# Performance work log

Measured on AMD Instinct MI355X. Metric: run time of the kernel, lower is better.

The kernel has to match this reference:

```python
import jax, jax.numpy as jnp
import numpy as np

B, S = 64, 32
C_IN, H, W = 4, 84, 84
D_MODEL, D_STATE, D_CONV, EXPAND = 128, 32, 4, 2
D_INNER = EXPAND * D_MODEL  # 256
DT_RANK = D_MODEL // 16     # 8
CNN_OUT = 64 * 7 * 7        # 3136
FC1, FC2, NA = 128, 128, 18


def setup_inputs() -> dict:
    key = jax.random.key(0)
    ks = jax.random.split(key, 24)
    def g(k, shape, scale=0.02):
        return jax.random.normal(k, shape, dtype=jnp.float32) * scale
    return {
        "x": jax.random.uniform(ks[0], (B, S, C_IN, H, W), dtype=jnp.float32) * 255.0,
        "conv1_w": g(ks[1], (32, C_IN, 8, 8)), "conv1_b": g(ks[2], (32,)),
        "conv2_w": g(ks[3], (64, 32, 4, 4)), "conv2_b": g(ks[4], (64,)),
        "conv3_w": g(ks[5], (64, 64, 3, 3)), "conv3_b": g(ks[6], (64,)),
        "feat_w": g(ks[7], (D_MODEL, CNN_OUT)), "feat_b": g(ks[8], (D_MODEL,)),
        "in_proj_w": g(ks[9], (2 * D_INNER, D_MODEL)),
        "conv1d_w": g(ks[10], (D_INNER, 1, D_CONV)), "conv1d_b": g(ks[11], (D_INNER,)),
        "x_proj_w": g(ks[12], (DT_RANK + 2 * D_STATE, D_INNER)),
        "dt_proj_w": g(ks[13], (D_INNER, DT_RANK), 0.1),
        "dt_proj_b": g(ks[14], (D_INNER,), 0.5),
        "A_log": jnp.log(jnp.tile(jnp.arange(1, D_STATE + 1, dtype=jnp.float32), (D_INNER, 1))),
        "D": jnp.ones((D_INNER,), jnp.float32),
        "out_proj_w": g(ks[15], (D_MODEL, D_INNER)),
        "fc1_w": g(ks[16], (FC1, D_MODEL)), "fc1_b": g(ks[17], (FC1,)),
        "fc2_w": g(ks[18], (FC2, FC1)), "fc2_b": g(ks[19], (FC2,)),
        "q_w": g(ks[20], (NA, FC2)), "q_b": g(ks[21], (NA,)),
    }


def _conv2d_relu(x, w, b, stride):
    y = jax.lax.conv_general_dilated(
        x, w, (stride, stride), 'VALID',
        dimension_numbers=('NCHW', 'OIHW', 'NCHW'))
    return jax.nn.relu(y + b[None, :, None, None])


def _mamba(x, in_proj_w, conv1d_w, conv1d_b, x_proj_w, dt_proj_w, dt_proj_b,
           A_log, Dvec, out_proj_w):
    # x: (B, L, d_model)
    Bb = x.shape[0]
    xz = x @ in_proj_w.T                      # (B,L,2*d_inner)
    u, z = jnp.split(xz, 2, axis=-1)
    # causal depthwise conv along L
    uc = jnp.transpose(u, (0, 2, 1))          # (B,d_inner,L)
    uc = jax.lax.conv_general_dilated(
        uc, conv1d_w, (1,), [(D_CONV - 1, 0)],
        dimension_numbers=('NCL', 'OIL', 'NCL'), feature_group_count=D_INNER)
    u = jax.nn.silu(jnp.transpose(uc, (0, 2, 1)) + conv1d_b)   # (B,L,d_inner)
    x_dbl = u @ x_proj_w.T                    # (B,L,dt_rank+2*d_state)
    dt, Bm, Cm = jnp.split(x_dbl, [DT_RANK, DT_RANK + D_STATE], axis=-1)
    dt = jax.nn.softplus(dt @ dt_proj_w.T + dt_proj_b)          # (B,L,d_inner)
    A = -jnp.exp(A_log)                       # (d_inner,d_state)
    dA = jnp.exp(dt[..., None] * A)           # (B,L,d_inner,d_state)
    dBu = dt[..., None] * Bm[:, :, None, :] * u[..., None]      # (B,L,d_inner,d_state)

    def step(h, inp):
        dA_t, dBu_t, C_t = inp
        h = dA_t * h + dBu_t                  # (B,d_inner,d_state)
        return h, jnp.einsum('bdn,bn->bd', h, C_t)

    h0 = jnp.zeros((Bb, D_INNER, D_STATE), x.dtype)
    _, ys = jax.lax.scan(step, h0,
                         (dA.swapaxes(0, 1), dBu.swapaxes(0, 1), Cm.swapaxes(0, 1)))
    y = ys.swapaxes(0, 1) + Dvec * u          # (B,L,d_inner)
    y = y * jax.nn.silu(z)
    return y @ out_proj_w.T                   # (B,L,d_model)


def reference(x, conv1_w, conv1_b, conv2_w, conv2_b, conv3_w, conv3_b,
              feat_w, feat_b, in_proj_w, conv1d_w, conv1d_b, x_proj_w,
              dt_proj_w, dt_proj_b, A_log, D, out_proj_w,
              fc1_w, fc1_b, fc2_w, fc2_b, q_w, q_b):
    Bn, Sn = x.shape[0], x.shape[1]
    xf = x.reshape(Bn * Sn, C_IN, H, W) / 255.0
    h = _conv2d_relu(xf, conv1_w, conv1_b, 4)   # (BS,32,20,20)
    h = _conv2d_relu(h, conv2_w, conv2_b, 2)    # (BS,64,9,9)
    h = _conv2d_relu(h, conv3_w, conv3_b, 1)    # (BS,64,7,7)
    h = h.reshape(Bn * Sn, -1)
    feat = h @ feat_w.T + feat_b                # (BS,d_model)
    seq = feat.reshape(Bn, Sn, D_MODEL)
    mo = _mamba(seq, in_proj_w, conv1d_w, conv1d_b, x_proj_w,
                dt_proj_w, dt_proj_b, A_log, D, out_proj_w)
    latent = mo[:, -1, :]                       # (B,d_model)
    hh = jax.nn.relu(latent @ fc1_w.T + fc1_b)
    hh = jax.nn.relu(hh @ fc2_w.T + fc2_b)
    q = hh @ q_w.T + q_b                        # (B,num_actions)
    return (q, latent)
```

## Files before the change

kernel.cpp:

```cpp
#include <hip/hip_runtime.h>
#include <math.h>

#define NIMG   2048
#define BATCH  64
#define SEQ    32

__device__ __forceinline__ float siluf(float v) { return v / (1.0f + expf(-v)); }
__device__ __forceinline__ float reluf(float v) { return v > 0.0f ? v : 0.0f; }
__device__ __forceinline__ float softplusf(float x) {
    return x > 0.0f ? x + log1pf(expf(-x)) : log1pf(expf(x));
}

__global__ __launch_bounds__(128) void k_conv1(const float* __restrict__ x,
                                               const float* __restrict__ w,
                                               const float* __restrict__ bias,
                                               float* __restrict__ out) {
    __shared__ float s_in[4][20][84];
    const int tid = threadIdx.x;
    const int img = blockIdx.x;
    const float* __restrict__ xin = x + (size_t)img * (4 * 84 * 84);

    const int ocg  = tid >> 4;
    const int rem  = tid & 15;
    const int oy_l = rem >> 2;
    const int oxg  = rem & 3;
    const int oc0  = ocg * 4;
    const int ox0  = oxg * 5;
    const int iy0  = oy_l * 4;

    float b0 = bias[oc0], b1 = bias[oc0 + 1], b2 = bias[oc0 + 2], b3 = bias[oc0 + 3];

    for (int chunk = 0; chunk < 5; ++chunk) {
        __syncthreads();
        const int row0 = chunk * 16;
        for (int i = tid; i < 4 * 20 * 84; i += 128) {
            int c = i / 1680, r = (i % 1680) / 84, col = i % 84;
            s_in[c][r][col] = xin[(size_t)(c * 84 + row0 + r) * 84 + col] * (1.0f / 255.0f);
        }
        __syncthreads();

        float acc[4][5];
        #pragma unroll
        for (int o = 0; o < 4; ++o)
            #pragma unroll
            for (int j = 0; j < 5; ++j) acc[o][j] = 0.0f;

        for (int ic = 0; ic < 4; ++ic) {
            #pragma unroll
            for (int ky = 0; ky < 8; ++ky) {
                const float* irow = &s_in[ic][iy0 + ky][0];
                float4 wa[4], wb[4];
                #pragma unroll
                for (int o = 0; o < 4; ++o) {
                    const float* wp = w + ((size_t)(oc0 + o) * 4 + ic) * 64 + ky * 8;
                    wa[o] = *(const float4*)wp;
                    wb[o] = *(const float4*)(wp + 4);
                }
                #pragma unroll
                for (int j = 0; j < 5; ++j) {
                    const float* ip = irow + (ox0 + j) * 4;
                    float4 ia = *(const float4*)ip;
                    float4 ib = *(const float4*)(ip + 4);
                    #pragma unroll
                    for (int o = 0; o < 4; ++o) {
                        acc[o][j] += wa[o].x * ia.x + wa[o].y * ia.y + wa[o].z * ia.z + wa[o].w * ia.w
                                   + wb[o].x * ib.x + wb[o].y * ib.y + wb[o].z * ib.z + wb[o].w * ib.w;
                    }
                }
            }
        }

        const int oy = chunk * 4 + oy_l;
        float bb[4] = {b0, b1, b2, b3};
        #pragma unroll
        for (int o = 0; o < 4; ++o)
            #pragma unroll
            for (int j = 0; j < 5; ++j)
                out[((size_t)img * 32 + oc0 + o) * 400 + oy * 20 + ox0 + j] = reluf(acc[o][j] + bb[o]);
    }
}

__global__ __launch_bounds__(320) void k_conv2(const float* __restrict__ in,
                                               const float* __restrict__ w,
                                               const float* __restrict__ bias,
                                               float* __restrict__ out) {
    __shared__ float s_in[32][20][20];
    const int tid = threadIdx.x;
    const int img = blockIdx.x;
    const float* __restrict__ src = in + (size_t)img * 12800;
    for (int i = tid; i < 3200; i += 320) ((float4*)s_in)[i] = ((const float4*)src)[i];
    __syncthreads();

    if (tid < 288) {
        const int ocg = tid / 9, oy = tid % 9;
        const int oc0 = ocg * 2;
        float acc0[9], acc1[9];
        #pragma unroll
        for (int j = 0; j < 9; ++j) { acc0[j] = 0.0f; acc1[j] = 0.0f; }

        for (int ic = 0; ic < 32; ++ic) {
            #pragma unroll
            for (int ky = 0; ky < 4; ++ky) {
                const float* irow = &s_in[ic][2 * oy + ky][0];
                float4 r0 = *(const float4*)(irow);
                float4 r1 = *(const float4*)(irow + 4);
                float4 r2 = *(const float4*)(irow + 8);
                float4 r3 = *(const float4*)(irow + 12);
                float4 r4 = *(const float4*)(irow + 16);
                float xr[20] = {r0.x, r0.y, r0.z, r0.w, r1.x, r1.y, r1.z, r1.w,
                                r2.x, r2.y, r2.z, r2.w, r3.x, r3.y, r3.z, r3.w,
                                r4.x, r4.y, r4.z, r4.w};
                const float* wp0 = w + ((size_t)oc0 * 32 + ic) * 16 + ky * 4;
                float4 w0 = *(const float4*)wp0;
                float4 w1 = *(const float4*)(wp0 + 32 * 16);
                #pragma unroll
                for (int ox = 0; ox < 9; ++ox) {
                    float i0 = xr[2 * ox], i1 = xr[2 * ox + 1], i2 = xr[2 * ox + 2], i3 = xr[2 * ox + 3];
                    acc0[ox] += w0.x * i0 + w0.y * i1 + w0.z * i2 + w0.w * i3;
                    acc1[ox] += w1.x * i0 + w1.y * i1 + w1.z * i2 + w1.w * i3;
                }
            }
        }
        float bb0 = bias[oc0], bb1 = bias[oc0 + 1];
        #pragma unroll
        for (int ox = 0; ox < 9; ++ox) {
            out[((size_t)img * 64 + oc0) * 81 + oy * 9 + ox]     = reluf(acc0[ox] + bb0);
            out[((size_t)img * 64 + oc0 + 1) * 81 + oy * 9 + ox] = reluf(acc1[ox] + bb1);
        }
    }
}

__global__ __launch_bounds__(256) void k_conv3(const float* __restrict__ in,
                                               const float* __restrict__ w,
                                               const float* __restrict__ bias,
                                               float* __restrict__ out) {
    __shared__ float s_in[64][81];
    const int tid = threadIdx.x;
    const int img = blockIdx.x;
    const float* __restrict__ src = in + (size_t)img * 5184;
    for (int i = tid; i < 1296; i += 256) ((float4*)s_in)[i] = ((const float4*)src)[i];
    __syncthreads();

    if (tid < 224) {
        const int ocg = tid / 7, oy = tid % 7;
        const int oc0 = ocg * 2;
        float acc0[7], acc1[7];
        #pragma unroll
        for (int j = 0; j < 7; ++j) { acc0[j] = 0.0f; acc1[j] = 0.0f; }

        for (int ic = 0; ic < 64; ++ic) {
            #pragma unroll
            for (int ky = 0; ky < 3; ++ky) {
                const float* irow = &s_in[ic][(oy + ky) * 9];
                float xr[9];
                #pragma unroll
                for (int t = 0; t < 9; ++t) xr[t] = irow[t];
                const float* wp0 = w + ((size_t)oc0 * 64 + ic) * 9 + ky * 3;
                const float* wp1 = wp0 + 64 * 9;
                float w00 = wp0[0], w01 = wp0[1], w02 = wp0[2];
                float w10 = wp1[0], w11 = wp1[1], w12 = wp1[2];
                #pragma unroll
                for (int ox = 0; ox < 7; ++ox) {
                    acc0[ox] += w00 * xr[ox] + w01 * xr[ox + 1] + w02 * xr[ox + 2];
                    acc1[ox] += w10 * xr[ox] + w11 * xr[ox + 1] + w12 * xr[ox + 2];
                }
            }
        }
        float bb0 = bias[oc0], bb1 = bias[oc0 + 1];
        #pragma unroll
        for (int ox = 0; ox < 7; ++ox) {
            out[(size_t)img * 3136 + oc0 * 49 + oy * 7 + ox]       = reluf(acc0[ox] + bb0);
            out[(size_t)img * 3136 + (oc0 + 1) * 49 + oy * 7 + ox] = reluf(acc1[ox] + bb1);
        }
    }
}

__global__ __launch_bounds__(256) void k_gemm(const float* __restrict__ A,
                                              const float* __restrict__ W,
                                              float* __restrict__ C,
                                              int M, int N, int K, int kpz) {
    __shared__ float As[16][68];
    __shared__ float Ws[16][68];
    const int tid = threadIdx.x;
    const int m0 = blockIdx.x * 64, n0 = blockIdx.y * 64;
    const int k0 = blockIdx.z * kpz;
    const int lr = tid >> 4, lc = tid & 15;
    const int tm = tid >> 4, tn = tid & 15;

    float acc[4][4];
    #pragma unroll
    for (int i = 0; i < 4; ++i)
        #pragma unroll
        for (int j = 0; j < 4; ++j) acc[i][j] = 0.0f;

    for (int kc = 0; kc < kpz; kc += 16) {
        const int kb = k0 + kc + lc;
        __syncthreads();
        #pragma unroll
        for (int i = 0; i < 4; ++i) {
            int r = lr + 16 * i;
            As[lc][r] = A[(size_t)(m0 + r) * K + kb];
            int wr = n0 + r;
            Ws[lc][r] = (wr < N) ? W[(size_t)wr * K + kb] : 0.0f;
        }
        __syncthreads();
        #pragma unroll
        for (int kk = 0; kk < 16; ++kk) {
            float4 a = *(const float4*)&As[kk][tm * 4];
            float4 b = *(const float4*)&Ws[kk][tn * 4];
            acc[0][0] += a.x * b.x; acc[0][1] += a.x * b.y; acc[0][2] += a.x * b.z; acc[0][3] += a.x * b.w;
            acc[1][0] += a.y * b.x; acc[1][1] += a.y * b.y; acc[1][2] += a.y * b.z; acc[1][3] += a.y * b.w;
            acc[2][0] += a.z * b.x; acc[2][1] += a.z * b.y; acc[2][2] += a.z * b.z; acc[2][3] += a.z * b.w;
            acc[3][0] += a.w * b.x; acc[3][1] += a.w * b.y; acc[3][2] += a.w * b.z; acc[3][3] += a.w * b.w;
        }
    }

    float* Cz = C + (size_t)blockIdx.z * M * N;
    #pragma unroll
    for (int i = 0; i < 4; ++i) {
        int m = m0 + tm * 4 + i;
        #pragma unroll
        for (int j = 0; j < 4; ++j) {
            int n = n0 + tn * 4 + j;
            if (n < N) Cz[(size_t)m * N + n] = acc[i][j];
        }
    }
}

__global__ __launch_bounds__(256) void k_reduce7(const float* __restrict__ P,
                                                 const float* __restrict__ bias,
                                                 float* __restrict__ out) {
    int idx = blockIdx.x * 256 + threadIdx.x;
    int n = idx & 127;
    float s = bias[n];
    #pragma unroll
    for (int z = 0; z < 7; ++z) s += P[(size_t)z * 2048 * 128 + idx];
    out[idx] = s;
}

__global__ __launch_bounds__(256) void k_conv1d(const float* __restrict__ xz,
                                                const float* __restrict__ w,
                                                const float* __restrict__ bias,
                                                float* __restrict__ u) {
    const int b = blockIdx.x, sg = blockIdx.y;
    const int d = threadIdx.x;
    const float w0 = w[d * 4], w1 = w[d * 4 + 1], w2 = w[d * 4 + 2], w3 = w[d * 4 + 3];
    const float bb = bias[d];
    const int s0 = sg * 8;
    float p1 = 0.0f, p2 = 0.0f, p3 = 0.0f;
    int sstart = (sg == 0) ? 0 : s0 - 3;
    for (int s = sstart; s < s0 + 8; ++s) {
        float cur = xz[(size_t)(b * 32 + s) * 512 + d];
        if (s >= s0) {
            float v = w0 * p3 + w1 * p2 + w2 * p1 + w3 * cur + bb;
            u[(size_t)(b * 32 + s) * 256 + d] = siluf(v);
        }
        p3 = p2; p2 = p1; p1 = cur;
    }
}

__global__ __launch_bounds__(256) void k_dtproj(const float* __restrict__ xdbl,
                                                const float* __restrict__ w,
                                                const float* __restrict__ bias,
                                                float* __restrict__ dt) {
    const int row = blockIdx.x;
    const int j = threadIdx.x;
    float r[8];
    #pragma unroll
    for (int k = 0; k < 8; ++k) r[k] = xdbl[(size_t)row * 72 + k];
    float acc = bias[j];
    #pragma unroll
    for (int k = 0; k < 8; ++k) acc += r[k] * w[j * 8 + k];
    dt[(size_t)row * 256 + j] = softplusf(acc);
}

__global__ __launch_bounds__(256) void k_scan(const float* __restrict__ xdbl,
                                              const float* __restrict__ dt,
                                              const float* __restrict__ u,
                                              const float* __restrict__ A_log,
                                              const float* __restrict__ Dv,
                                              const float* __restrict__ xz,
                                              float* __restrict__ ylast) {
    const int blk = blockIdx.x;
    const int b = blk >> 5, dg = blk & 31;
    const int lane = threadIdx.x & 63;
    const int wv = threadIdx.x >> 6;
    const int n = lane & 31;
    const int d = dg * 8 + wv * 2 + (lane >> 5);

    const float A = -expf(A_log[d * 32 + n]);
    float h = 0.0f;
    const size_t rowbase = (size_t)b * 32;
    for (int s = 0; s < 32; ++s) {
        size_t r = rowbase + s;
        float dtv = dt[r * 256 + d];
        float Bn  = xdbl[r * 72 + 8 + n];
        float uv  = u[r * 256 + d];
        float dA  = expf(dtv * A);
        h = dA * h + dtv * Bn * uv;
    }
    size_t r31 = rowbase + 31;
    float yv = h * xdbl[r31 * 72 + 40 + n];
    #pragma unroll
    for (int off = 16; off > 0; off >>= 1) yv += __shfl_xor(yv, off);
    if (n == 0) {
        float uv31 = u[r31 * 256 + d];
        float y = yv + Dv[d] * uv31;
        float z = xz[r31 * 512 + 256 + d];
        ylast[b * 256 + d] = y * siluf(z);
    }
}

__global__ __launch_bounds__(128) void k_head(const float* __restrict__ ylast,
                                              const float* __restrict__ op_w,
                                              const float* __restrict__ fc1_w,
                                              const float* __restrict__ fc1_b,
                                              const float* __restrict__ fc2_w,
                                              const float* __restrict__ fc2_b,
                                              const float* __restrict__ q_w,
                                              const float* __restrict__ q_b,
                                              float* __restrict__ out) {
    __shared__ float s_y[256];
    __shared__ float s_l[128];
    __shared__ float s_h1[128];
    __shared__ float s_h2[128];
    const int b = blockIdx.x;
    const int j = threadIdx.x;
    s_y[j]       = ylast[b * 256 + j];
    s_y[j + 128] = ylast[b * 256 + 128 + j];
    __syncthreads();

    {
        float acc = 0.0f;
        const float* wr = op_w + (size_t)j * 256;
        for (int k = 0; k < 256; k += 4) {
            float4 wv = *(const float4*)(wr + k);
            acc += wv.x * s_y[k] + wv.y * s_y[k + 1] + wv.z * s_y[k + 2] + wv.w * s_y[k + 3];
        }
        s_l[j] = acc;
        out[1152 + b * 128 + j] = acc;
    }
    __syncthreads();
    {
        float acc = fc1_b[j];
        const float* wr = fc1_w + (size_t)j * 128;
        for (int k = 0; k < 128; k += 4) {
            float4 wv = *(const float4*)(wr + k);
            acc += wv.x * s_l[k] + wv.y * s_l[k + 1] + wv.z * s_l[k + 2] + wv.w * s_l[k + 3];
        }
        s_h1[j] = reluf(acc);
    }
    __syncthreads();
    {
        float acc = fc2_b[j];
        const float* wr = fc2_w + (size_t)j * 128;
        for (int k = 0; k < 128; k += 4) {
            float4 wv = *(const float4*)(wr + k);
            acc += wv.x * s_h1[k] + wv.y * s_h1[k + 1] + wv.z * s_h1[k + 2] + wv.w * s_h1[k + 3];
        }
        s_h2[j] = reluf(acc);
    }
    __syncthreads();
    if (j < 18) {
        float acc = q_b[j];
        const float* wr = q_w + (size_t)j * 128;
        for (int k = 0; k < 128; k += 4) {
            float4 wv = *(const float4*)(wr + k);
            acc += wv.x * s_h2[k] + wv.y * s_h2[k + 1] + wv.z * s_h2[k + 2] + wv.w * s_h2[k + 3];
        }
        out[b * 18 + j] = acc;
    }
}

extern "C" void kernel_launch(void* const* d_in, const int* in_sizes, int n_in,
                              void* d_out, int out_size, void* d_ws, size_t ws_size,
                              hipStream_t stream) {
    const float* x        = (const float*)d_in[0];
    const float* conv1_w  = (const float*)d_in[1];
    const float* conv1_b  = (const float*)d_in[2];
    const float* conv2_w  = (const float*)d_in[3];
    const float* conv2_b  = (const float*)d_in[4];
    const float* conv3_w  = (const float*)d_in[5];
    const float* conv3_b  = (const float*)d_in[6];
    const float* feat_w   = (const float*)d_in[7];
    const float* feat_b   = (const float*)d_in[8];
    const float* in_proj_w = (const float*)d_in[9];
    const float* conv1d_w = (const float*)d_in[10];
    const float* conv1d_b = (const float*)d_in[11];
    const float* x_proj_w = (const float*)d_in[12];
    const float* dt_proj_w = (const float*)d_in[13];
    const float* dt_proj_b = (const float*)d_in[14];
    const float* A_log    = (const float*)d_in[15];
    const float* Dvec     = (const float*)d_in[16];
    const float* out_proj_w = (const float*)d_in[17];
    const float* fc1_w    = (const float*)d_in[18];
    const float* fc1_b    = (const float*)d_in[19];
    const float* fc2_w    = (const float*)d_in[20];
    const float* fc2_b    = (const float*)d_in[21];
    const float* q_w      = (const float*)d_in[22];
    const float* q_b      = (const float*)d_in[23];
    float* out = (float*)d_out;

    float* ws = (float*)d_ws;
    float* c1    = ws;
    float* c2    = ws + 26214400;
    float* c3    = ws;
    float* featP = ws + 6422528;
    float* feat  = ws + 8257536;
    float* xz    = ws + 8519680;
    float* u     = ws + 9568256;
    float* xdbl  = ws + 10092544;
    float* dt    = ws + 10240000;
    float* ylast = ws + 10764288;

    k_conv1<<<dim3(NIMG), dim3(128), 0, stream>>>(x, conv1_w, conv1_b, c1);
    k_conv2<<<dim3(NIMG), dim3(320), 0, stream>>>(c1, conv2_w, conv2_b, c2);
    k_conv3<<<dim3(NIMG), dim3(256), 0, stream>>>(c2, conv3_w, conv3_b, c3);

    k_gemm<<<dim3(32, 2, 7), dim3(256), 0, stream>>>(c3, feat_w, featP, 2048, 128, 3136, 448);
    k_reduce7<<<dim3(1024), dim3(256), 0, stream>>>(featP, feat_b, feat);

    k_gemm<<<dim3(32, 8, 1), dim3(256), 0, stream>>>(feat, in_proj_w, xz, 2048, 512, 128, 128);

    k_conv1d<<<dim3(64, 4), dim3(256), 0, stream>>>(xz, conv1d_w, conv1d_b, u);

    k_gemm<<<dim3(32, 2, 1), dim3(256), 0, stream>>>(u, x_proj_w, xdbl, 2048, 72, 256, 256);

    k_dtproj<<<dim3(2048), dim3(256), 0, stream>>>(xdbl, dt_proj_w, dt_proj_b, dt);

    k_scan<<<dim3(2048), dim3(256), 0, stream>>>(xdbl, dt, u, A_log, Dvec, xz, ylast);

    k_head<<<dim3(64), dim3(128), 0, stream>>>(ylast, out_proj_w, fc1_w, fc1_b,
                                               fc2_w, fc2_b, q_w, q_b, out);
}
```

Measured before the change: 1.398 ms.

## Retile the three conv kernels for more outputs per thread and split conv1 rows

conv1 now splits each image into four row chunks across blockIdx.y, loads input with float4, and keeps a 24-wide input row in registers that is reused across four output channels. conv2 and conv3 each have threads compute four output channels instead of two, using smaller blocks with launch-bounds occupancy hints. conv3's shared tile is padded to 12 columns so rows can be read as float4. The aim is fewer redundant shared-memory reads per FMA and better parallelism for conv1, at the cost of higher register pressure and idle threads in every block.

```diff
diff --git a/kernel.cpp b/kernel.cpp
--- a/kernel.cpp
+++ b/kernel.cpp
@@ -11,33 +11,35 @@
     return x > 0.0f ? x + log1pf(expf(-x)) : log1pf(expf(x));
 }
 
-__global__ __launch_bounds__(128) void k_conv1(const float* __restrict__ x,
-                                               const float* __restrict__ w,
-                                               const float* __restrict__ bias,
-                                               float* __restrict__ out) {
-    __shared__ float s_in[4][20][84];
+__global__ __launch_bounds__(192, 3) void k_conv1(const float* __restrict__ x,
+                                                  const float* __restrict__ w,
+                                                  const float* __restrict__ bias,
+                                                  float* __restrict__ out) {
+    __shared__ float s_in[4][24][84];
     const int tid = threadIdx.x;
     const int img = blockIdx.x;
+    const int chunk = blockIdx.y;
     const float* __restrict__ xin = x + (size_t)img * (4 * 84 * 84);
-
-    const int ocg  = tid >> 4;
-    const int rem  = tid & 15;
-    const int oy_l = rem >> 2;
-    const int oxg  = rem & 3;
-    const int oc0  = ocg * 4;
-    const int ox0  = oxg * 5;
-    const int iy0  = oy_l * 4;
-
-    float b0 = bias[oc0], b1 = bias[oc0 + 1], b2 = bias[oc0 + 2], b3 = bias[oc0 + 3];
-
-    for (int chunk = 0; chunk < 5; ++chunk) {
-        __syncthreads();
-        const int row0 = chunk * 16;
-        for (int i = tid; i < 4 * 20 * 84; i += 128) {
-            int c = i / 1680, r = (i % 1680) / 84, col = i % 84;
-            s_in[c][r][col] = xin[(size_t)(c * 84 + row0 + r) * 84 + col] * (1.0f / 255.0f);
-        }
-        __syncthreads();
+    const int row0 = chunk * 20;
+
+    for (int i = tid; i < 2016; i += 192) {
+        int ic = i / 504, rem = i % 504;
+        int r = rem / 21, c4 = rem % 21;
+        float4 v = *(const float4*)&xin[(size_t)(ic * 84 + row0 + r) * 84 + c4 * 4];
+        v.x *= (1.0f / 255.0f); v.y *= (1.0f / 255.0f);
+        v.z *= (1.0f / 255.0f); v.w *= (1.0f / 255.0f);
+        *(float4*)&s_in[ic][r][c4 * 4] = v;
+    }
+    __syncthreads();
+
+    if (tid < 160) {
+        const int ocg = tid / 20;
+        const int pix = tid % 20;
+        const int oy_l = pix / 4;
+        const int oxg  = pix % 4;
+        const int oc0 = ocg * 4;
+        const int iy0 = oy_l * 4;
+        const int col0 = oxg * 20;
 
         float acc[4][5];
         #pragma unroll
@@ -48,129 +50,146 @@
         for (int ic = 0; ic < 4; ++ic) {
             #pragma unroll
             for (int ky = 0; ky < 8; ++ky) {
-                const float* irow = &s_in[ic][iy0 + ky][0];
-                float4 wa[4], wb[4];
+                const float* irow = &s_in[ic][iy0 + ky][col0];
+                float xr[24];
+                #pragma unroll
+                for (int t = 0; t < 6; ++t) {
+                    float4 v = *(const float4*)(irow + t * 4);
+                    xr[t * 4] = v.x; xr[t * 4 + 1] = v.y; xr[t * 4 + 2] = v.z; xr[t * 4 + 3] = v.w;
+                }
                 #pragma unroll
                 for (int o = 0; o < 4; ++o) {
                     const float* wp = w + ((size_t)(oc0 + o) * 4 + ic) * 64 + ky * 8;
-                    wa[o] = *(const float4*)wp;
-                    wb[o] = *(const float4*)(wp + 4);
-                }
-                #pragma unroll
-                for (int j = 0; j < 5; ++j) {
-                    const float* ip = irow + (ox0 + j) * 4;
-                    float4 ia = *(const float4*)ip;
-                    float4 ib = *(const float4*)(ip + 4);
+                    float4 wa = *(const float4*)wp;
+                    float4 wb = *(const float4*)(wp + 4);
                     #pragma unroll
-                    for (int o = 0; o < 4; ++o) {
-                        acc[o][j] += wa[o].x * ia.x + wa[o].y * ia.y + wa[o].z * ia.z + wa[o].w * ia.w
-                                   + wb[o].x * ib.x + wb[o].y * ib.y + wb[o].z * ib.z + wb[o].w * ib.w;
+                    for (int j = 0; j < 5; ++j) {
+                        const float* xp = &xr[j * 4];
+                        acc[o][j] += wa.x * xp[0] + wa.y * xp[1] + wa.z * xp[2] + wa.w * xp[3]
+                                   + wb.x * xp[4] + wb.y * xp[5] + wb.z * xp[6] + wb.w * xp[7];
                     }
                 }
             }
         }
 
-        const int oy = chunk * 4 + oy_l;
-        float bb[4] = {b0, b1, b2, b3};
-        #pragma unroll
-        for (int o = 0; o < 4; ++o)
+        const int oy = chunk * 5 + oy_l;
+        #pragma unroll
+        for (int o = 0; o < 4; ++o) {
+            float bb = bias[oc0 + o];
             #pragma unroll
             for (int j = 0; j < 5; ++j)
-                out[((size_t)img * 32 + oc0 + o) * 400 + oy * 20 + ox0 + j] = reluf(acc[o][j] + bb[o]);
-    }
-}
-
-__global__ __launch_bounds__(320) void k_conv2(const float* __restrict__ in,
-                                               const float* __restrict__ w,
-                                               const float* __restrict__ bias,
-                                               float* __restrict__ out) {
+                out[((size_t)img * 32 + oc0 + o) * 400 + oy * 20 + oxg * 5 + j] = reluf(acc[o][j] + bb);
+        }
+    }
+}
+
+__global__ __launch_bounds__(192, 2) void k_conv2(const float* __restrict__ in,
+                                                  const float* __restrict__ w,
+                                                  const float* __restrict__ bias,
+                                                  float* __restrict__ out) {
     __shared__ float s_in[32][20][20];
     const int tid = threadIdx.x;
     const int img = blockIdx.x;
     const float* __restrict__ src = in + (size_t)img * 12800;
-    for (int i = tid; i < 3200; i += 320) ((float4*)s_in)[i] = ((const float4*)src)[i];
-    __syncthreads();
-
-    if (tid < 288) {
+    for (int i = tid; i < 3200; i += 192) ((float4*)s_in)[i] = ((const float4*)src)[i];
+    __syncthreads();
+
+    if (tid < 144) {
         const int ocg = tid / 9, oy = tid % 9;
-        const int oc0 = ocg * 2;
-        float acc0[9], acc1[9];
-        #pragma unroll
-        for (int j = 0; j < 9; ++j) { acc0[j] = 0.0f; acc1[j] = 0.0f; }
+        const int oc0 = ocg * 4;
+        float acc[4][9];
+        #pragma unroll
+        for (int o = 0; o < 4; ++o)
+            #pragma unroll
+            for (int j = 0; j < 9; ++j) acc[o][j] = 0.0f;
 
         for (int ic = 0; ic < 32; ++ic) {
             #pragma unroll
             for (int ky = 0; ky < 4; ++ky) {
                 const float* irow = &s_in[ic][2 * oy + ky][0];
-                float4 r0 = *(const float4*)(irow);
-                float4 r1 = *(const float4*)(irow + 4);
-                float4 r2 = *(const float4*)(irow + 8);
-                float4 r3 = *(const float4*)(irow + 12);
-                float4 r4 = *(const float4*)(irow + 16);
-                float xr[20] = {r0.x, r0.y, r0.z, r0.w, r1.x, r1.y, r1.z, r1.w,
-                                r2.x, r2.y, r2.z, r2.w, r3.x, r3.y, r3.z, r3.w,
-                                r4.x, r4.y, r4.z, r4.w};
-                const float* wp0 = w + ((size_t)oc0 * 32 + ic) * 16 + ky * 4;
-                float4 w0 = *(const float4*)wp0;
-                float4 w1 = *(const float4*)(wp0 + 32 * 16);
-                #pragma unroll
-                for (int ox = 0; ox < 9; ++ox) {
-                    float i0 = xr[2 * ox], i1 = xr[2 * ox + 1], i2 = xr[2 * ox + 2], i3 = xr[2 * ox + 3];
-                    acc0[ox] += w0.x * i0 + w0.y * i1 + w0.z * i2 + w0.w * i3;
-                    acc1[ox] += w1.x * i0 + w1.y * i1 + w1.z * i2 + w1.w * i3;
+                float xr[20];
+                #pragma unroll
+                for (int t = 0; t < 5; ++t) {
+                    float4 v = *(const float4*)(irow + t * 4);
+                    xr[t * 4] = v.x; xr[t * 4 + 1] = v.y; xr[t * 4 + 2] = v.z; xr[t * 4 + 3] = v.w;
+                }
+                #pragma unroll
+                for (int o = 0; o < 4; ++o) {
+                    float4 wv = *(const float4*)(w + ((size_t)(oc0 + o) * 32 + ic) * 16 + ky * 4);
+                    #pragma unroll
+                    for (int ox = 0; ox < 9; ++ox) {
+                        acc[o][ox] += wv.x * xr[2 * ox] + wv.y * xr[2 * ox + 1]
+                                    + wv.z * xr[2 * ox + 2] + wv.w * xr[2 * ox + 3];
+                    }
                 }
             }
         }
-        float bb0 = bias[oc0], bb1 = bias[oc0 + 1];
-        #pragma unroll
-        for (int ox = 0; ox < 9; ++ox) {
-            out[((size_t)img * 64 + oc0) * 81 + oy * 9 + ox]     = reluf(acc0[ox] + bb0);
-            out[((size_t)img * 64 + oc0 + 1) * 81 + oy * 9 + ox] = reluf(acc1[ox] + bb1);
-        }
-    }
-}
-
-__global__ __launch_bounds__(256) void k_conv3(const float* __restrict__ in,
-                                               const float* __restrict__ w,
-                                               const float* __restrict__ bias,
-                                               float* __restrict__ out) {
-    __shared__ float s_in[64][81];
+        #pragma unroll
+        for (int o = 0; o < 4; ++o) {
+            float bb = bias[oc0 + o];
+            #pragma unroll
+            for (int ox = 0; ox < 9; ++ox)
+                out[((size_t)img * 64 + oc0 + o) * 81 + oy * 9 + ox] = reluf(acc[o][ox] + bb);
+        }
+    }
+}
+
+__global__ __launch_bounds__(128, 2) void k_conv3(const float* __restrict__ in,
+                                                  const float* __restrict__ w,
+                                                  const float* __restrict__ bias,
+                                                  float* __restrict__ out) {
+    __shared__ float s_in[64][9][12];
     const int tid = threadIdx.x;
     const int img = blockIdx.x;
     const float* __restrict__ src = in + (size_t)img * 5184;
-    for (int i = tid; i < 1296; i += 256) ((float4*)s_in)[i] = ((const float4*)src)[i];
-    __syncthreads();
-
-    if (tid < 224) {
+    for (int i = tid; i < 1296; i += 128) {
+        float4 v = ((const float4*)src)[i];
+        int base = i * 4;
+        #pragma unroll
+        for (int e = 0; e < 4; ++e) {
+            int idx = base + e;
+            int ic = idx / 81, rem = idx % 81;
+            float val = (e == 0) ? v.x : (e == 1) ? v.y : (e == 2) ? v.z : v.w;
+            s_in[ic][rem / 9][rem % 9] = val;
+        }
+    }
+    __syncthreads();
+
+    if (tid < 112) {
         const int ocg = tid / 7, oy = tid % 7;
-        const int oc0 = ocg * 2;
-        float acc0[7], acc1[7];
-        #pragma unroll
-        for (int j = 0; j < 7; ++j) { acc0[j] = 0.0f; acc1[j] = 0.0f; }
+        const int oc0 = ocg * 4;
+        float acc[4][7];
+        #pragma unroll
+        for (int o = 0; o < 4; ++o)
+            #pragma unroll
+            for (int j = 0; j < 7; ++j) acc[o][j] = 0.0f;
 
         for (int ic = 0; ic < 64; ++ic) {
             #pragma unroll
             for (int ky = 0; ky < 3; ++ky) {
-                const float* irow = &s_in[ic][(oy + ky) * 9];
-                float xr[9];
-                #pragma unroll
-                for (int t = 0; t < 9; ++t) xr[t] = irow[t];
-                const float* wp0 = w + ((size_t)oc0 * 64 + ic) * 9 + ky * 3;
-                const float* wp1 = wp0 + 64 * 9;
-                float w00 = wp0[0], w01 = wp0[1], w02 = wp0[2];
-                float w10 = wp1[0], w11 = wp1[1], w12 = wp1[2];
-                #pragma unroll
-                for (int ox = 0; ox < 7; ++ox) {
-                    acc0[ox] += w00 * xr[ox] + w01 * xr[ox + 1] + w02 * xr[ox + 2];
-                    acc1[ox] += w10 * xr[ox] + w11 * xr[ox + 1] + w12 * xr[ox + 2];
+                const float* irow = &s_in[ic][oy + ky][0];
+                float xr[12];
+                #pragma unroll
+                for (int t = 0; t < 3; ++t) {
+                    float4 v = *(const float4*)(irow + t * 4);
+                    xr[t * 4] = v.x; xr[t * 4 + 1] = v.y; xr[t * 4 + 2] = v.z; xr[t * 4 + 3] = v.w;
+                }
+                #pragma unroll
+                for (int o = 0; o < 4; ++o) {
+                    const float* wp = w + ((size_t)(oc0 + o) * 64 + ic) * 9 + ky * 3;
+                    float w0 = wp[0], w1 = wp[1], w2 = wp[2];
+                    #pragma unroll
+                    for (int ox = 0; ox < 7; ++ox)
+                        acc[o][ox] += w0 * xr[ox] + w1 * xr[ox + 1] + w2 * xr[ox + 2];
                 }
             }
         }
-        float bb0 = bias[oc0], bb1 = bias[oc0 + 1];
-        #pragma unroll
-        for (int ox = 0; ox < 7; ++ox) {
-            out[(size_t)img * 3136 + oc0 * 49 + oy * 7 + ox]       = reluf(acc0[ox] + bb0);
-            out[(size_t)img * 3136 + (oc0 + 1) * 49 + oy * 7 + ox] = reluf(acc1[ox] + bb1);
+        #pragma unroll
+        for (int o = 0; o < 4; ++o) {
+            float bb = bias[oc0 + o];
+            #pragma unroll
+            for (int ox = 0; ox < 7; ++ox)
+                out[(size_t)img * 3136 + (oc0 + o) * 49 + oy * 7 + ox] = reluf(acc[o][ox] + bb);
         }
     }
 }
@@ -413,23 +432,18 @@
     float* dt    = ws + 10240000;
     float* ylast = ws + 10764288;
 
-    k_conv1<<<dim3(NIMG), dim3(128), 0, stream>>>(x, conv1_w, conv1_b, c1);
-    k_conv2<<<dim3(NIMG), dim3(320), 0, stream>>>(c1, conv2_w, conv2_b, c2);
-    k_conv3<<<dim3(NIMG), dim3(256), 0, stream>>>(c2, conv3_w, conv3_b, c3);
+    k_conv1<<<dim3(NIMG, 4), dim3(192), 0, stream>>>(x, conv1_w, conv1_b, c1);
+    k_conv2<<<dim3(NIMG), dim3(192), 0, stream>>>(c1, conv2_w, conv2_b, c2);
+    k_conv3<<<dim3(NIMG), dim3(128), 0, stream>>>(c2, conv3_w, conv3_b, c3);
 
     k_gemm<<<dim3(32, 2, 7), dim3(256), 0, stream>>>(c3, feat_w, featP, 2048, 128, 3136, 448);
     k_reduce7<<<dim3(1024), dim3(256), 0, stream>>>(featP, feat_b, feat);
 
     k_gemm<<<dim3(32, 8, 1), dim3(256), 0, stream>>>(feat, in_proj_w, xz, 2048, 512, 128, 128);
-
     k_conv1d<<<dim3(64, 4), dim3(256), 0, stream>>>(xz, conv1d_w, conv1d_b, u);
-
     k_gemm<<<dim3(32, 2, 1), dim3(256), 0, stream>>>(u, x_proj_w, xdbl, 2048, 72, 256, 256);
-
     k_dtproj<<<dim3(2048), dim3(256), 0, stream>>>(xdbl, dt_proj_w, dt_proj_b, dt);
-
     k_scan<<<dim3(2048), dim3(256), 0, stream>>>(xdbl, dt, u, A_log, Dvec, xz, ylast);
-
     k_head<<<dim3(64), dim3(128), 0, stream>>>(ylast, out_proj_w, fc1_w, fc1_b,
                                                fc2_w, fc2_b, q_w, q_b, out);
 }
```

Measured after the change: 4.775 ms. 3.42x slower.
